# Optimization experiments

Hardware: AMD Instinct MI355X
Metric: run time of the kernel (lower is better)

## Reference

```python
import jax, jax.numpy as jnp
import numpy as np

BS, N, F, R, OUT = 8, 512, 512, 16, 512
ALPHA = 0.2

def setup_inputs() -> dict:
    key = jax.random.key(0)
    ks = jax.random.split(key, 16)
    w = lambda k, shp: (jax.random.normal(k, shp, dtype=jnp.float32) * 0.05)
    return {
        'x_ori': jax.random.normal(ks[0], (BS, N, F), dtype=jnp.float32),
        'x': jax.random.normal(ks[1], (BS, N, F), dtype=jnp.float32),
        'c': jax.random.normal(ks[2], (BS, 1, F), dtype=jnp.float32),
        'adj': jax.random.randint(ks[3], (BS, N, N, R), 0, 2, dtype=jnp.int32),
        'Wfc': w(ks[4], (F, F)),
        'Wdc': w(ks[5], (F, F)),
        'Wqv': w(ks[6], (2 * F, F)),
        'Wkv': w(ks[7], (2 * F, F)),
        'Wqc': w(ks[8], (F, F)),
        'Wkc': w(ks[9], (F, F)),
        'Wa': w(ks[10], (2 * F, R)),
        'Wu': w(ks[11], (2 * F, OUT)),
    }

def reference(x_ori, x, c, adj, Wfc, Wdc, Wqv, Wkv, Wqc, Wkc, Wa, Wu):
    # relation-context modulation vector m: [bs,1,F]
    m = jnp.matmul(jax.nn.elu(jnp.matmul(c, Wfc)), Wdc)
    nodes = jnp.concatenate([x, x_ori], axis=2)          # [bs,N,2F]
    xq = jnp.matmul(nodes, Wqv) * jnp.matmul(m, Wqc)     # [bs,N,F]
    xk = jnp.matmul(nodes, Wkv) * jnp.matmul(m, Wkc)     # [bs,N,F]
    # scores[b,i,j,r] = leakyrelu(xq_i . Wa[:F,r] + xk_j . Wa[F:,r])
    # (equivalent to cat([xq_i,xk_j]) @ Wa without materializing [bs,N,N,2F])
    sq = jnp.matmul(xq, Wa[:F])                          # [bs,N,R]
    sk = jnp.matmul(xk, Wa[F:])                          # [bs,N,R]
    scores = jax.nn.leaky_relu(sq[:, :, None, :] + sk[:, None, :, :], ALPHA)
    adj_f = adj.astype(scores.dtype)                     # [bs,N,N,R]
    s = jnp.sum(scores * adj_f, axis=3)                  # [bs,N,N]
    mask = jnp.sum(adj_f, axis=3) > 0
    attn = jax.nn.softmax(jnp.where(mask, s, jnp.float32(-9e15)), axis=2)
    new_x = jnp.matmul(attn, x)                          # [bs,N,F]
    return jnp.matmul(jnp.concatenate([x, new_x], axis=2), Wu)
```

## Files before the change

### kernel.cpp

```cpp
#include <hip/hip_runtime.h>
#include <hip/hip_bf16.h>
#include <cstddef>
#include <cstdint>

static constexpr int BSZ  = 8;
static constexpr int NN   = 512;
static constexpr int FF   = 512;
static constexpr int RR   = 16;
static constexpr int TWOF = 1024;

typedef __attribute__((ext_vector_type(8))) short short8;
typedef __attribute__((ext_vector_type(4))) float f32x4;

__device__ __forceinline__ ushort bf16_bits(float v) {
    union { __hip_bfloat16 h; ushort u; } cvt;
    cvt.h = __float2bfloat16(v);
    return cvt.u;
}

static constexpr size_t OFF_TB     = 0;
static constexpr size_t OFF_MB     = 16384;
static constexpr size_t OFF_MQ     = 32768;
static constexpr size_t OFF_MK     = 49152;
static constexpr size_t OFF_SQ     = 65536;
static constexpr size_t OFF_SK     = 327680;
static constexpr size_t OFF_WQET   = 589824;
static constexpr size_t OFF_WKET   = 851968;
static constexpr size_t OFF_XBF    = 5308416;
static constexpr size_t OFF_XTBF   = 9502720;
static constexpr size_t OFF_XORIBF = 13697024;
static constexpr size_t OFF_NEWXBF = 17891328;
static constexpr size_t OFF_WUT    = 22085632;

__global__ __launch_bounds__(256) void k_prep(
    const float* __restrict__ x_ori, const float* __restrict__ x,
    const float* __restrict__ c, const float* __restrict__ Wfc,
    const float* __restrict__ Wu,
    ushort* __restrict__ xori_bf, ushort* __restrict__ x_bf,
    ushort* __restrict__ xT_bf, ushort* __restrict__ WuT,
    float* __restrict__ tb)
{
    int blk = blockIdx.x;
    int t = threadIdx.x;
    if (blk < 1024) {
        int idx = blk * 256 + t;
        float4 a = ((const float4*)x_ori)[idx * 2];
        float4 b = ((const float4*)x_ori)[idx * 2 + 1];
        uint4 s;
        s.x = (uint)bf16_bits(a.x) | ((uint)bf16_bits(a.y) << 16);
        s.y = (uint)bf16_bits(a.z) | ((uint)bf16_bits(a.w) << 16);
        s.z = (uint)bf16_bits(b.x) | ((uint)bf16_bits(b.y) << 16);
        s.w = (uint)bf16_bits(b.z) | ((uint)bf16_bits(b.w) << 16);
        ((uint4*)xori_bf)[idx] = s;
    } else if (blk < 3072) {
        __shared__ float tile[32][33];
        int bb = blk - 1024;
        int f0 = (bb & 15) * 32, i0 = ((bb >> 4) & 15) * 32, b = bb >> 8;
        int c2 = (t & 15) * 2, r = t >> 4;
#pragma unroll
        for (int rr = 0; rr < 32; rr += 16) {
            int i = i0 + r + rr;
            const float* xp = &x[((size_t)b * NN + i) * FF + f0 + c2];
            float v0 = xp[0], v1 = xp[1];
            tile[r + rr][c2] = v0;
            tile[r + rr][c2 + 1] = v1;
            *(uint*)&x_bf[((size_t)b * NN + i) * FF + f0 + c2] =
                (uint)bf16_bits(v0) | ((uint)bf16_bits(v1) << 16);
        }
        __syncthreads();
#pragma unroll
        for (int ff = 0; ff < 32; ff += 16) {
            int f = f0 + r + ff;
            *(uint*)&xT_bf[((size_t)b * FF + f) * NN + i0 + c2] =
                (uint)bf16_bits(tile[c2][r + ff]) |
                ((uint)bf16_bits(tile[c2 + 1][r + ff]) << 16);
        }
    } else if (blk < 3584) {
        __shared__ float tile2[32][33];
        int bb = blk - 3072;
        int f0 = (bb & 31) * 32, o0 = (bb >> 5) * 32;
        int cc = t & 31, r0 = t >> 5;
#pragma unroll
        for (int rr = 0; rr < 32; rr += 8)
            tile2[r0 + rr][cc] = Wu[(size_t)(f0 + r0 + rr) * FF + o0 + cc];
        __syncthreads();
#pragma unroll
        for (int rr = 0; rr < 32; rr += 8)
            WuT[(size_t)(o0 + r0 + rr) * TWOF + f0 + cc] = bf16_bits(tile2[cc][r0 + rr]);
    } else {
        __shared__ float red1[8][32];
        int bb = blk - 3584;
        int b = bb >> 4, f0 = (bb & 15) * 32;
        int f = t & 31, kq = t >> 5;
        const float* vb = c + (size_t)b * FF;
        float acc = 0.f;
        int ks = kq * 64;
#pragma unroll 8
        for (int k = ks; k < ks + 64; ++k)
            acc = fmaf(vb[k], Wfc[(size_t)k * FF + f0 + f], acc);
        red1[kq][f] = acc;
        __syncthreads();
        if (kq == 0) {
            acc += red1[1][f] + red1[2][f] + red1[3][f] + red1[4][f] +
                   red1[5][f] + red1[6][f] + red1[7][f];
            tb[(size_t)b * FF + f0 + f] = (acc > 0.f) ? acc : expm1f(acc);
        }
    }
}

__global__ __launch_bounds__(256) void k_matvec(const float* __restrict__ vin,
                                                const float* __restrict__ W,
                                                float* __restrict__ vout) {
    __shared__ float red[8][32];
    int b = blockIdx.y;
    int f0 = blockIdx.x * 32;
    int t = threadIdx.x;
    int f = t & 31, kq = t >> 5;
    const float* vb = vin + (size_t)b * FF;
    float acc = 0.f;
    int ks = kq * 64;
#pragma unroll 8
    for (int k = ks; k < ks + 64; ++k)
        acc = fmaf(vb[k], W[(size_t)k * FF + f0 + f], acc);
    red[kq][f] = acc;
    __syncthreads();
    if (kq == 0) {
        acc += red[1][f] + red[2][f] + red[3][f] + red[4][f] +
               red[5][f] + red[6][f] + red[7][f];
        vout[(size_t)b * FF + f0 + f] = acc;
    }
}

__global__ __launch_bounds__(256) void k_mqk(const float* __restrict__ m,
                                             const float* __restrict__ Wqc,
                                             const float* __restrict__ Wkc,
                                             float* __restrict__ mq,
                                             float* __restrict__ mk) {
    __shared__ float redq[8][32];
    __shared__ float redk[8][32];
    int b = blockIdx.y;
    int f0 = blockIdx.x * 32;
    int t = threadIdx.x;
    int f = t & 31, kq = t >> 5;
    const float* mb = m + (size_t)b * FF;
    float aq = 0.f, ak = 0.f;
    int ks = kq * 64;
#pragma unroll 8
    for (int k = ks; k < ks + 64; ++k) {
        float mv = mb[k];
        aq = fmaf(mv, Wqc[(size_t)k * FF + f0 + f], aq);
        ak = fmaf(mv, Wkc[(size_t)k * FF + f0 + f], ak);
    }
    redq[kq][f] = aq;
    redk[kq][f] = ak;
    __syncthreads();
    if (kq == 0) {
        aq += redq[1][f] + redq[2][f] + redq[3][f] + redq[4][f] +
              redq[5][f] + redq[6][f] + redq[7][f];
        ak += redk[1][f] + redk[2][f] + redk[3][f] + redk[4][f] +
              redk[5][f] + redk[6][f] + redk[7][f];
        mq[(size_t)b * FF + f0 + f] = aq;
        mk[(size_t)b * FF + f0 + f] = ak;
    }
}

__global__ __launch_bounds__(256) void k_weff(const float* __restrict__ Wqv,
                                              const float* __restrict__ Wkv,
                                              const float* __restrict__ Wa,
                                              const float* __restrict__ mqv,
                                              const float* __restrict__ mkv,
                                              ushort* __restrict__ WqEt,
                                              ushort* __restrict__ WkEt) {
    int z = blockIdx.z;
    const float* W = z ? Wkv : Wqv;
    const float* mvec = z ? mkv : mqv;
    ushort* WeffT = z ? WkEt : WqEt;
    int waRowOff = z ? FF : 0;

    __shared__ float4 wa4[FF * 4];
    int tid = threadIdx.x;
    int b = blockIdx.y;
    const float* mv = mvec + (size_t)b * FF;
#pragma unroll
    for (int qq = 0; qq < 8; ++qq) {
        int idx = tid + qq * 256;
        int f = idx >> 2, rq = idx & 3;
        float4 w = *reinterpret_cast<const float4*>(Wa + (size_t)(waRowOff + f) * RR + rq * 4);
        float s = mv[f];
        float4 o;
        o.x = w.x * s; o.y = w.y * s; o.z = w.z * s; o.w = w.w * s;
        wa4[idx] = o;
    }
    __syncthreads();
    int k_l = tid >> 2, r4 = tid & 3;
    int k = blockIdx.x * 64 + k_l;
    const float4* Wrow4 = reinterpret_cast<const float4*>(W + (size_t)k * FF);
    float4 acc = {0.f, 0.f, 0.f, 0.f};
#pragma unroll 4
    for (int f4 = 0; f4 < FF / 4; ++f4) {
        float4 w = Wrow4[f4];
        float4 v0 = wa4[(f4 * 4 + 0) * 4 + r4];
        float4 v1 = wa4[(f4 * 4 + 1) * 4 + r4];
        float4 v2 = wa4[(f4 * 4 + 2) * 4 + r4];
        float4 v3 = wa4[(f4 * 4 + 3) * 4 + r4];
        acc.x = fmaf(w.x, v0.x, acc.x); acc.y = fmaf(w.x, v0.y, acc.y);
        acc.z = fmaf(w.x, v0.z, acc.z); acc.w = fmaf(w.x, v0.w, acc.w);
        acc.x = fmaf(w.y, v1.x, acc.x); acc.y = fmaf(w.y, v1.y, acc.y);
        acc.z = fmaf(w.y, v1.z, acc.z); acc.w = fmaf(w.y, v1.w, acc.w);
        acc.x = fmaf(w.z, v2.x, acc.x); acc.y = fmaf(w.z, v2.y, acc.y);
        acc.z = fmaf(w.z, v2.z, acc.z); acc.w = fmaf(w.z, v2.w, acc.w);
        acc.x = fmaf(w.w, v3.x, acc.x); acc.y = fmaf(w.w, v3.y, acc.y);
        acc.z = fmaf(w.w, v3.z, acc.z); acc.w = fmaf(w.w, v3.w, acc.w);
    }
    WeffT[((size_t)b * RR + r4 * 4 + 0) * TWOF + k] = bf16_bits(acc.x);
    WeffT[((size_t)b * RR + r4 * 4 + 1) * TWOF + k] = bf16_bits(acc.y);
    WeffT[((size_t)b * RR + r4 * 4 + 2) * TWOF + k] = bf16_bits(acc.z);
    WeffT[((size_t)b * RR + r4 * 4 + 3) * TWOF + k] = bf16_bits(acc.w);
}

__global__ __launch_bounds__(256) void k_sqsk(const ushort* __restrict__ x_bf,
                                              const ushort* __restrict__ xori_bf,
                                              const ushort* __restrict__ WqEt,
                                              const ushort* __restrict__ WkEt,
                                              float* __restrict__ sq,
                                              float* __restrict__ sk) {
    int t = threadIdx.x;
    int b = blockIdx.y;
    int m0 = blockIdx.x * 32;
    int lane = t & 63, w = t >> 6;
    int sub = w & 1, isK = w >> 1;
    int m_l = lane & 15, q = lane >> 4;
    int row = m0 + sub * 16 + m_l;
    const ushort* Bt = (isK ? WkEt : WqEt) + ((size_t)b * RR + m_l) * TWOF;
    f32x4 acc = {0.f, 0.f, 0.f, 0.f};
#pragma unroll
    for (int k0 = 0; k0 < TWOF; k0 += 32) {
        const ushort* src = (k0 < FF) ? x_bf : xori_bf;
        int kc = k0 & (FF - 1);
        short8 af = *(const short8*)(src + ((size_t)b * NN + row) * FF + kc + q * 8);
        short8 bf = *(const short8*)(Bt + k0 + q * 8);
        acc = __builtin_amdgcn_mfma_f32_16x16x32_bf16(af, bf, acc, 0, 0, 0);
    }
    float* dst = isK ? sk : sq;
#pragma unroll
    for (int r = 0; r < 4; ++r) {
        int i = m0 + sub * 16 + q * 4 + r;
        dst[((size_t)b * NN + i) * RR + m_l] = acc[r];
    }
}

__global__ __launch_bounds__(256, 2) void k_attn_pv(const int* __restrict__ adj,
                                                    const float* __restrict__ sq,
                                                    const float* __restrict__ sk,
                                                    const ushort* __restrict__ xT_bf,
                                                    ushort* __restrict__ newx_bf) {
    constexpr int ZS = 520;
    __shared__ ushort P[16 * ZS];
    __shared__ ushort mask_lds[16 * NN];
    __shared__ float  rowsum[16];
    int t = threadIdx.x;
    int b = blockIdx.y;
    int m0 = blockIdx.x * 16;

    {
        const int4* a4 = (const int4*)adj + ((size_t)b * NN + m0) * (NN * RR / 4);
        uint* ml = (uint*)mask_lds;
#pragma unroll 8
        for (int it = 0; it < 128; ++it) {
            int4 v = a4[it * 256 + t];
            uint bits = (uint)v.x | ((uint)v.y << 1) | ((uint)v.z << 2) | ((uint)v.w << 3);
            uint mp = bits << ((t & 3) * 4);
            mp |= (uint)__shfl_xor((int)mp, 1, 64);
            mp |= (uint)__shfl_xor((int)mp, 2, 64);
            uint hi = (uint)__shfl_xor((int)mp, 4, 64);
            if ((t & 7) == 0) {
                int p = (it * 256 + t) >> 2;
                ml[p >> 1] = (mp & 0xFFFFu) | (hi << 16);
            }
        }
    }
    __syncthreads();

    {
        int r = t >> 4, cc = t & 15;
        int i = m0 + r;
        const float4* sqp = (const float4*)(sq + ((size_t)b * NN + i) * RR);
        float4 q0 = sqp[0], q1 = sqp[1], q2 = sqp[2], q3 = sqp[3];
        float sv[16] = {q0.x, q0.y, q0.z, q0.w, q1.x, q1.y, q1.z, q1.w,
                        q2.x, q2.y, q2.z, q2.w, q3.x, q3.y, q3.z, q3.w};
        float z[32];
#pragma unroll 4
        for (int it = 0; it < 32; ++it) {
            int j = it * 16 + cc;
            uint mk = mask_lds[r * NN + j];
            const float4* kp = (const float4*)(sk + ((size_t)b * NN + j) * RR);
            float4 s0 = kp[0], s1 = kp[1], s2 = kp[2], s3 = kp[3];
            float ks[16] = {s0.x, s0.y, s0.z, s0.w, s1.x, s1.y, s1.z, s1.w,
                            s2.x, s2.y, s2.z, s2.w, s3.x, s3.y, s3.z, s3.w};
            float ssum = 0.f;
#pragma unroll
            for (int ridx = 0; ridx < 16; ++ridx) {
                float v_ = sv[ridx] + ks[ridx];
                v_ = fmaxf(v_, 0.2f * v_);
                ssum = fmaf(v_, (float)((mk >> ridx) & 1u), ssum);
            }
            z[it] = mk ? ssum : -9e15f;
        }
        float mx = z[0];
#pragma unroll
        for (int it = 1; it < 32; ++it) mx = fmaxf(mx, z[it]);
#pragma unroll
        for (int off = 1; off < 16; off <<= 1) mx = fmaxf(mx, __shfl_xor(mx, off, 64));
        float sum = 0.f;
        ushort* pr = &P[r * ZS];
#pragma unroll
        for (int it = 0; it < 32; ++it) {
            float e = __expf(z[it] - mx);
            pr[it * 16 + cc] = bf16_bits(e);
            sum += e;
        }
#pragma unroll
        for (int off = 1; off < 16; off <<= 1) sum += __shfl_xor(sum, off, 64);
        if (cc == 0) rowsum[r] = sum;
    }
    __syncthreads();

    {
        int w = t >> 6, lane = t & 63;
        int m_l = lane & 15, q = lane >> 4;
        int n0w = w * 128;
        f32x4 acc[8] = {};
        const ushort* xTb = xT_bf + (size_t)b * FF * NN;
        for (int k0 = 0; k0 < NN; k0 += 32) {
            short8 af = *(const short8*)(&P[m_l * ZS + k0 + q * 8]);
#pragma unroll
            for (int nb = 0; nb < 8; ++nb) {
                int n = n0w + nb * 16 + m_l;
                short8 bfr = *(const short8*)(xTb + (size_t)n * NN + k0 + q * 8);
                acc[nb] = __builtin_amdgcn_mfma_f32_16x16x32_bf16(af, bfr, acc[nb], 0, 0, 0);
            }
        }
        float inv[4];
#pragma unroll
        for (int rg = 0; rg < 4; ++rg) inv[rg] = 1.f / rowsum[q * 4 + rg];
#pragma unroll
        for (int nb = 0; nb < 8; ++nb) {
#pragma unroll
            for (int rg = 0; rg < 4; ++rg) {
                int i = m0 + q * 4 + rg;
                int f = n0w + nb * 16 + m_l;
                newx_bf[((size_t)b * NN + i) * FF + f] = bf16_bits(acc[nb][rg] * inv[rg]);
            }
        }
    }
}

__global__ __launch_bounds__(256) void k_gemm(const ushort* __restrict__ A1, size_t sA1,
                                              const ushort* __restrict__ A2, size_t sA2,
                                              const ushort* __restrict__ BT, size_t sBT,
                                              float* __restrict__ Cf, size_t sC,
                                              int K, int ldBT) {
    __shared__ ushort As[2][64 * 40];
    __shared__ ushort Bs[2][64 * 40];
    int t = threadIdx.x;
    int n0 = blockIdx.x * 64, m0 = blockIdx.y * 64, b = blockIdx.z;
    int row = t >> 2, c8 = (t & 3) * 8;
    int lane = t & 63, w = t >> 6;
    int m_l = lane & 15, q = lane >> 4;
    f32x4 acc[4] = {{0.f,0.f,0.f,0.f},{0.f,0.f,0.f,0.f},{0.f,0.f,0.f,0.f},{0.f,0.f,0.f,0.f}};
    const ushort* BTb = BT + (size_t)b * sBT;
    for (int k0 = 0; k0 < K; k0 += 64) {
#pragma unroll
        for (int h = 0; h < 2; ++h) {
            int kk = k0 + h * 32;
            const ushort* Aab; int kc;
            if (kk < FF) { Aab = A1 + (size_t)b * sA1; kc = kk; }
            else         { Aab = A2 + (size_t)b * sA2; kc = kk - FF; }
            uint4 av = *(const uint4*)(Aab + (size_t)(m0 + row) * FF + kc + c8);
            uint4 bv = *(const uint4*)(BTb + (size_t)(n0 + row) * ldBT + kk + c8);
            *(uint4*)(&As[h][row * 40 + c8]) = av;
            *(uint4*)(&Bs[h][row * 40 + c8]) = bv;
        }
        __syncthreads();
#pragma unroll
        for (int h = 0; h < 2; ++h) {
            short8 af = *(const short8*)(&As[h][(w * 16 + m_l) * 40 + q * 8]);
#pragma unroll
            for (int nb = 0; nb < 4; ++nb) {
                short8 bfr = *(const short8*)(&Bs[h][(nb * 16 + m_l) * 40 + q * 8]);
                acc[nb] = __builtin_amdgcn_mfma_f32_16x16x32_bf16(af, bfr, acc[nb], 0, 0, 0);
            }
        }
        __syncthreads();
    }
#pragma unroll
    for (int nb = 0; nb < 4; ++nb) {
#pragma unroll
        for (int r = 0; r < 4; ++r) {
            int mi = m0 + w * 16 + q * 4 + r;
            int ni = n0 + nb * 16 + m_l;
            Cf[(size_t)b * sC + (size_t)mi * FF + ni] = acc[nb][r];
        }
    }
}

extern "C" void kernel_launch(void* const* d_in, const int* in_sizes, int n_in,
                              void* d_out, int out_size, void* d_ws, size_t ws_size,
                              hipStream_t stream) {
    const float* x_ori = (const float*)d_in[0];
    const float* x     = (const float*)d_in[1];
    const float* c     = (const float*)d_in[2];
    const int*   adj   = (const int*)d_in[3];
    const float* Wfc   = (const float*)d_in[4];
    const float* Wdc   = (const float*)d_in[5];
    const float* Wqv   = (const float*)d_in[6];
    const float* Wkv   = (const float*)d_in[7];
    const float* Wqc   = (const float*)d_in[8];
    const float* Wkc   = (const float*)d_in[9];
    const float* Wa    = (const float*)d_in[10];
    const float* Wu    = (const float*)d_in[11];
    float* out = (float*)d_out;

    char* ws = (char*)d_ws;
    float*  tb      = (float*)(ws + OFF_TB);
    float*  mb      = (float*)(ws + OFF_MB);
    float*  mq      = (float*)(ws + OFF_MQ);
    float*  mk      = (float*)(ws + OFF_MK);
    float*  sq      = (float*)(ws + OFF_SQ);
    float*  sk      = (float*)(ws + OFF_SK);
    ushort* WqEt    = (ushort*)(ws + OFF_WQET);
    ushort* WkEt    = (ushort*)(ws + OFF_WKET);
    ushort* x_bf    = (ushort*)(ws + OFF_XBF);
    ushort* xT_bf   = (ushort*)(ws + OFF_XTBF);
    ushort* xori_bf = (ushort*)(ws + OFF_XORIBF);
    ushort* newx_bf = (ushort*)(ws + OFF_NEWXBF);
    ushort* WuT     = (ushort*)(ws + OFF_WUT);

    dim3 blk(256);

    k_prep<<<dim3(3712), blk, 0, stream>>>(x_ori, x, c, Wfc, Wu,
                                           xori_bf, x_bf, xT_bf, WuT, tb);

    k_matvec<<<dim3(16, BSZ), blk, 0, stream>>>(tb, Wdc, mb);
    k_mqk<<<dim3(16, BSZ), blk, 0, stream>>>(mb, Wqc, Wkc, mq, mk);

    k_weff<<<dim3(16, BSZ, 2), blk, 0, stream>>>(Wqv, Wkv, Wa, mq, mk, WqEt, WkEt);

    k_sqsk<<<dim3(16, BSZ), blk, 0, stream>>>(x_bf, xori_bf, WqEt, WkEt, sq, sk);

    k_attn_pv<<<dim3(32, BSZ), blk, 0, stream>>>(adj, sq, sk, xT_bf, newx_bf);

    k_gemm<<<dim3(8, 8, BSZ), blk, 0, stream>>>(
        x_bf, (size_t)NN * FF, newx_bf, (size_t)NN * FF,
        WuT, (size_t)0, out, (size_t)NN * FF, TWOF, TWOF);
}
```

Before: 362.3 us.

## Split masked score computation into a separate wide-grid kernel before softmax-PV

The adjacency read and masked leaky-relu score reduction move out of the attention kernel into a new k_scores kernel launched over 4096 blocks per the whole problem. It writes a float score matrix to workspace, which k_attn_pv then reads for softmax and the PV matmul. Before, only 256 blocks streamed the 128MB adj tensor, which likely left bandwidth underused. The cost is an extra 8MB round-trip of scores through global memory and one more launch.

```diff
diff --git a/kernel.cpp b/kernel.cpp
--- a/kernel.cpp
+++ b/kernel.cpp
@@ -31,6 +31,7 @@
 static constexpr size_t OFF_XORIBF = 13697024;
 static constexpr size_t OFF_NEWXBF = 17891328;
 static constexpr size_t OFF_WUT    = 22085632;
+static constexpr size_t OFF_Z      = 23134208;
 
 __global__ __launch_bounds__(256) void k_prep(
     const float* __restrict__ x_ori, const float* __restrict__ x,
@@ -249,73 +250,70 @@
     }
 }
 
-__global__ __launch_bounds__(256, 2) void k_attn_pv(const int* __restrict__ adj,
-                                                    const float* __restrict__ sq,
-                                                    const float* __restrict__ sk,
-                                                    const ushort* __restrict__ xT_bf,
-                                                    ushort* __restrict__ newx_bf) {
+__global__ __launch_bounds__(256) void k_scores(const int* __restrict__ adj,
+                                                const float* __restrict__ sq,
+                                                const float* __restrict__ sk,
+                                                float* __restrict__ z) {
+    int b = blockIdx.z;
+    int i0 = blockIdx.y * 4;
+    int j0 = blockIdx.x * 128;
+    int t = threadIdx.x;
+    int jj = t & 127, rg = (t >> 7) * 2;
+    int j = j0 + jj;
+    const float4* kp = (const float4*)(sk + ((size_t)b * NN + j) * RR);
+    float4 s0 = kp[0], s1 = kp[1], s2 = kp[2], s3 = kp[3];
+    float ks[16] = {s0.x, s0.y, s0.z, s0.w, s1.x, s1.y, s1.z, s1.w,
+                    s2.x, s2.y, s2.z, s2.w, s3.x, s3.y, s3.z, s3.w};
+#pragma unroll
+    for (int r = 0; r < 2; ++r) {
+        int i = i0 + rg + r;
+        const int4* ap = (const int4*)(adj + (((size_t)b * NN + i) * NN + j) * RR);
+        int4 a0 = ap[0], a1 = ap[1], a2 = ap[2], a3 = ap[3];
+        const float4* qp = (const float4*)(sq + ((size_t)b * NN + i) * RR);
+        float4 q0 = qp[0], q1 = qp[1], q2 = qp[2], q3 = qp[3];
+        float sv[16] = {q0.x, q0.y, q0.z, q0.w, q1.x, q1.y, q1.z, q1.w,
+                        q2.x, q2.y, q2.z, q2.w, q3.x, q3.y, q3.z, q3.w};
+        int av[16] = {a0.x, a0.y, a0.z, a0.w, a1.x, a1.y, a1.z, a1.w,
+                      a2.x, a2.y, a2.z, a2.w, a3.x, a3.y, a3.z, a3.w};
+        int any = 0;
+        float ssum = 0.f;
+#pragma unroll
+        for (int ridx = 0; ridx < 16; ++ridx) {
+            float v_ = sv[ridx] + ks[ridx];
+            v_ = fmaxf(v_, 0.2f * v_);
+            ssum = fmaf(v_, (float)av[ridx], ssum);
+            any |= av[ridx];
+        }
+        z[((size_t)b * NN + i) * NN + j] = any ? ssum : -9e15f;
+    }
+}
+
+__global__ __launch_bounds__(256) void k_attn_pv(const float* __restrict__ z,
+                                                 const ushort* __restrict__ xT_bf,
+                                                 ushort* __restrict__ newx_bf) {
     constexpr int ZS = 520;
     __shared__ ushort P[16 * ZS];
-    __shared__ ushort mask_lds[16 * NN];
     __shared__ float  rowsum[16];
     int t = threadIdx.x;
     int b = blockIdx.y;
     int m0 = blockIdx.x * 16;
 
     {
-        const int4* a4 = (const int4*)adj + ((size_t)b * NN + m0) * (NN * RR / 4);
-        uint* ml = (uint*)mask_lds;
-#pragma unroll 8
-        for (int it = 0; it < 128; ++it) {
-            int4 v = a4[it * 256 + t];
-            uint bits = (uint)v.x | ((uint)v.y << 1) | ((uint)v.z << 2) | ((uint)v.w << 3);
-            uint mp = bits << ((t & 3) * 4);
-            mp |= (uint)__shfl_xor((int)mp, 1, 64);
-            mp |= (uint)__shfl_xor((int)mp, 2, 64);
-            uint hi = (uint)__shfl_xor((int)mp, 4, 64);
-            if ((t & 7) == 0) {
-                int p = (it * 256 + t) >> 2;
-                ml[p >> 1] = (mp & 0xFFFFu) | (hi << 16);
-            }
-        }
-    }
-    __syncthreads();
-
-    {
         int r = t >> 4, cc = t & 15;
-        int i = m0 + r;
-        const float4* sqp = (const float4*)(sq + ((size_t)b * NN + i) * RR);
-        float4 q0 = sqp[0], q1 = sqp[1], q2 = sqp[2], q3 = sqp[3];
-        float sv[16] = {q0.x, q0.y, q0.z, q0.w, q1.x, q1.y, q1.z, q1.w,
-                        q2.x, q2.y, q2.z, q2.w, q3.x, q3.y, q3.z, q3.w};
-        float z[32];
-#pragma unroll 4
-        for (int it = 0; it < 32; ++it) {
-            int j = it * 16 + cc;
-            uint mk = mask_lds[r * NN + j];
-            const float4* kp = (const float4*)(sk + ((size_t)b * NN + j) * RR);
-            float4 s0 = kp[0], s1 = kp[1], s2 = kp[2], s3 = kp[3];
-            float ks[16] = {s0.x, s0.y, s0.z, s0.w, s1.x, s1.y, s1.z, s1.w,
-                            s2.x, s2.y, s2.z, s2.w, s3.x, s3.y, s3.z, s3.w};
-            float ssum = 0.f;
-#pragma unroll
-            for (int ridx = 0; ridx < 16; ++ridx) {
-                float v_ = sv[ridx] + ks[ridx];
-                v_ = fmaxf(v_, 0.2f * v_);
-                ssum = fmaf(v_, (float)((mk >> ridx) & 1u), ssum);
-            }
-            z[it] = mk ? ssum : -9e15f;
-        }
-        float mx = z[0];
-#pragma unroll
-        for (int it = 1; it < 32; ++it) mx = fmaxf(mx, z[it]);
+        const float* zr = z + ((size_t)b * NN + m0 + r) * NN;
+        float zv[32];
+#pragma unroll
+        for (int it = 0; it < 32; ++it) zv[it] = zr[it * 16 + cc];
+        float mx = zv[0];
+#pragma unroll
+        for (int it = 1; it < 32; ++it) mx = fmaxf(mx, zv[it]);
 #pragma unroll
         for (int off = 1; off < 16; off <<= 1) mx = fmaxf(mx, __shfl_xor(mx, off, 64));
         float sum = 0.f;
         ushort* pr = &P[r * ZS];
 #pragma unroll
         for (int it = 0; it < 32; ++it) {
-            float e = __expf(z[it] - mx);
+            float e = __expf(zv[it] - mx);
             pr[it * 16 + cc] = bf16_bits(e);
             sum += e;
         }
@@ -435,6 +433,7 @@
     ushort* xori_bf = (ushort*)(ws + OFF_XORIBF);
     ushort* newx_bf = (ushort*)(ws + OFF_NEWXBF);
     ushort* WuT     = (ushort*)(ws + OFF_WUT);
+    float*  zbuf    = (float*)(ws + OFF_Z);
 
     dim3 blk(256);
 
@@ -448,7 +447,9 @@
 
     k_sqsk<<<dim3(16, BSZ), blk, 0, stream>>>(x_bf, xori_bf, WqEt, WkEt, sq, sk);
 
-    k_attn_pv<<<dim3(32, BSZ), blk, 0, stream>>>(adj, sq, sk, xT_bf, newx_bf);
+    k_scores<<<dim3(4, 128, BSZ), blk, 0, stream>>>(adj, sq, sk, zbuf);
+
+    k_attn_pv<<<dim3(32, BSZ), blk, 0, stream>>>(zbuf, xT_bf, newx_bf);
 
     k_gemm<<<dim3(8, 8, BSZ), blk, 0, stream>>>(
         x_bf, (size_t)NN * FF, newx_bf, (size_t)NN * FF,
```

Measured after the change: 308.7 us. 1.17x faster.
